# Performance work log

Measured on AMD Instinct MI355X. Metric: run time of the kernel, lower is better.

The kernel has to match this reference:

```python
import jax, jax.numpy as jnp
import numpy as np

B, S, D, H = 4, 1024, 1024, 16
DK = D // H  # f_out = 64


def setup_inputs() -> dict:
    key = jax.random.key(0)
    ks = jax.random.split(key, 20)
    sc = 0.02
    inp = {
        "q": jax.random.normal(ks[0], (B, S, D), jnp.float32),
        "k": jax.random.normal(ks[1], (B, S, D), jnp.float32),
        "v": jax.random.normal(ks[2], (B, S, D), jnp.float32),
        "mask": jnp.ones((B * H, S), jnp.int32),
        # q_lin / k_lin / v_lin: Linear(num_hiddens=D, num_q=D)
        "Wq": jax.random.normal(ks[3], (D, D), jnp.float32) * sc,
        "bq": jnp.zeros((D,), jnp.float32),
        "Wk": jax.random.normal(ks[4], (D, D), jnp.float32) * sc,
        "bk": jnp.zeros((D,), jnp.float32),
        "Wv": jax.random.normal(ks[5], (D, D), jnp.float32) * sc,
        "bv": jnp.zeros((D,), jnp.float32),
        # per-head FeedForward (Linear f_out->f_out + ReLU; dropout is a no-op in eval)
        "Wqf": jax.random.normal(ks[6], (DK, DK), jnp.float32) * sc,
        "bqf": jnp.zeros((DK,), jnp.float32),
        "Wkf": jax.random.normal(ks[7], (DK, DK), jnp.float32) * sc,
        "bkf": jnp.zeros((DK,), jnp.float32),
        "Wvf": jax.random.normal(ks[8], (DK, DK), jnp.float32) * sc,
        "bvf": jnp.zeros((DK,), jnp.float32),
        # out: Linear(f_out, f_out), applied per head before recombining
        "Wo": jax.random.normal(ks[9], (DK, DK), jnp.float32) * sc,
        "bo": jnp.zeros((DK,), jnp.float32),
    }
    return inp


def reference(q, k, v, mask, Wq, bq, Wk, bk, Wv, bv,
              Wqf, bqf, Wkf, bkf, Wvf, bvf, Wo, bo):
    def lin(x, W, b):
        return jnp.einsum("...i,oi->...o", x, W) + b

    def split_heads(x):  # (B,S,D) -> (B*H,S,DK)
        return x.reshape(B, S, H, DK).transpose(0, 2, 1, 3).reshape(B * H, S, DK)

    # projections + head split + per-head FeedForward (Linear -> ReLU)
    Q = jax.nn.relu(lin(split_heads(lin(q, Wq, bq)), Wqf, bqf))
    K = jax.nn.relu(lin(split_heads(lin(k, Wk, bk)), Wkf, bkf))
    V = jax.nn.relu(lin(split_heads(lin(v, Wv, bv)), Wvf, bvf))

    # scaled dot-product attention with padding mask (dropout = identity, eval)
    scores = jnp.einsum("bqd,bkd->bqk", Q, K) / np.sqrt(DK).astype(np.float32)
    scores = jnp.where(mask[:, None, :] == 0, -10000.0, scores)
    attn = jax.nn.softmax(scores, axis=-1)
    out = jnp.einsum("bqk,bkd->bqd", attn, V)  # (B*H,S,DK)

    out = lin(out, Wo, bo)  # per-head output projection (DK -> DK)
    # transpose_output: (B*H,S,DK) -> (B,S,H*DK)
    out = out.reshape(B, H, S, DK).transpose(0, 2, 1, 3).reshape(B, S, H * DK)
    return out
```

## Files before the change

### kernel.cpp

```cpp
#include <hip/hip_runtime.h>
#include <stdint.h>

#define MM 4096
#define SS 1024
#define DD 1024
#define HH 16
#define DKK 64

typedef __bf16 bf16x8 __attribute__((ext_vector_type(8)));
typedef __bf16 bf16x4 __attribute__((ext_vector_type(4)));
typedef float  f32x4  __attribute__((ext_vector_type(4)));

__device__ __forceinline__ void gload_lds16(const void* g, void* l) {
  __builtin_amdgcn_global_load_lds(
      (__attribute__((address_space(1))) void*)g,
      (__attribute__((address_space(3))) void*)l, 16, 0, 0);
}

#define LSW(row, ch) ((row) * 64 + ((((ch) ^ ((row) & 7)) << 3)))

__global__ __launch_bounds__(256) void prep(
    const float* __restrict__ q, const float* __restrict__ k,
    const float* __restrict__ v,
    const float* __restrict__ Wq, const float* __restrict__ bq,
    const float* __restrict__ Wk, const float* __restrict__ bk,
    const float* __restrict__ Wv, const float* __restrict__ bv,
    const float* __restrict__ Wqf, const float* __restrict__ bqf,
    const float* __restrict__ Wkf, const float* __restrict__ bkf,
    const float* __restrict__ Wvf, const float* __restrict__ bvf,
    __bf16* __restrict__ X3, __bf16* __restrict__ Wc3,
    float* __restrict__ bc3) {
  int blk = blockIdx.x;
  if (blk < 6144) {
    int z = blk >> 11;
    int bx = blk & 2047;
    const float* src = (z == 0) ? q : ((z == 1) ? k : v);
    size_t i = ((size_t)bx * 256 + threadIdx.x) * 8;
    float4 a = *(const float4*)(src + i);
    float4 b = *(const float4*)(src + i + 4);
    bf16x8 r;
    r[0] = (__bf16)a.x; r[1] = (__bf16)a.y; r[2] = (__bf16)a.z; r[3] = (__bf16)a.w;
    r[4] = (__bf16)b.x; r[5] = (__bf16)b.y; r[6] = (__bf16)b.z; r[7] = (__bf16)b.w;
    *(bf16x8*)(X3 + (size_t)z * MM * DD + i) = r;
  } else {
    int t = blk - 6144;
    int z = t >> 12;
    int wb = t & 4095;
    int i = (wb & 3) * 256 + threadIdx.x;
    int o = wb >> 2;
    const float* W   = (z == 0) ? Wq  : ((z == 1) ? Wk  : Wv);
    const float* bs  = (z == 0) ? bq  : ((z == 1) ? bk  : bv);
    const float* Wf  = (z == 0) ? Wqf : ((z == 1) ? Wkf : Wvf);
    const float* bf_ = (z == 0) ? bqf : ((z == 1) ? bkf : bvf);
    int h = o >> 6, j = o & 63;
    const float* wfr = Wf + j * DKK;
    float acc = 0.f;
#pragma unroll 8
    for (int d = 0; d < DKK; ++d)
      acc += wfr[d] * W[(size_t)(h * DKK + d) * DD + i];
    Wc3[(size_t)z * DD * DD + (size_t)o * DD + i] = (__bf16)acc;
    if ((wb & 3) == 0 && threadIdx.x == 0) {
      float bb = bf_[j];
      for (int d = 0; d < DKK; ++d) bb += wfr[d] * bs[h * DKK + d];
      bc3[z * DD + o] = bb;
    }
  }
}

__global__ __launch_bounds__(256) void gemm3(const __bf16* __restrict__ X3,
                                             const __bf16* __restrict__ Wc3,
                                             const float* __restrict__ bc3,
                                             __bf16* __restrict__ QKV) {
  __shared__ __bf16 As[128 * 64];
  __shared__ __bf16 Bs[128 * 64];
  const int z = blockIdx.z;
  const __bf16* A  = X3  + (size_t)z * MM * DD;
  const __bf16* Bt = Wc3 + (size_t)z * DD * DD;
  const float* bias = bc3 + z * DD;
  __bf16* C = QKV + (size_t)z * MM * DD;

  const int tid = threadIdx.x;
  const int wave = tid >> 6, lane = tid & 63;
  const int l15 = lane & 15, l4 = lane >> 4;
  const int bm = blockIdx.x * 128;
  const int bn = blockIdx.y * 128;
  const int wr = (wave >> 1) * 64;
  const int wc = (wave & 1) * 64;

  f32x4 acc[4][4] = {};

  const int srow = wave * 8 + (lane >> 3);
  const int scol = (lane & 7) * 8;

  for (int kt = 0; kt < DD; kt += 64) {
    __syncthreads();
#pragma unroll
    for (int j = 0; j < 4; ++j) {
      int row = j * 32 + srow;
      gload_lds16(A  + (size_t)(bm + row) * DD + kt + scol, As + j * 2048 + wave * 512);
      gload_lds16(Bt + (size_t)(bn + row) * DD + kt + scol, Bs + j * 2048 + wave * 512);
    }
    asm volatile("s_waitcnt vmcnt(0)" ::: "memory");
    __syncthreads();
#pragma unroll
    for (int ks = 0; ks < 2; ++ks) {
      bf16x8 af[4], bfr[4];
#pragma unroll
      for (int mi = 0; mi < 4; ++mi)
        af[mi] = *(const bf16x8*)(As + (wr + mi * 16 + l15) * 64 + ks * 32 + l4 * 8);
#pragma unroll
      for (int ni = 0; ni < 4; ++ni)
        bfr[ni] = *(const bf16x8*)(Bs + (wc + ni * 16 + l15) * 64 + ks * 32 + l4 * 8);
#pragma unroll
      for (int mi = 0; mi < 4; ++mi)
#pragma unroll
        for (int ni = 0; ni < 4; ++ni)
          acc[mi][ni] = __builtin_amdgcn_mfma_f32_16x16x32_bf16(af[mi], bfr[ni], acc[mi][ni], 0, 0, 0);
    }
  }

#pragma unroll
  for (int ni = 0; ni < 4; ++ni) {
    int n = bn + wc + ni * 16 + l15;
    float bb = bias[n];
#pragma unroll
    for (int mi = 0; mi < 4; ++mi) {
      if (z != 2) {
#pragma unroll
        for (int r = 0; r < 4; ++r) {
          int m = bm + wr + mi * 16 + l4 * 4 + r;
          float vv = acc[mi][ni][r] + bb;
          vv = vv > 0.f ? vv : 0.f;
          C[(size_t)m * DD + n] = (__bf16)vv;
        }
      } else {
        int m0 = bm + wr + mi * 16 + l4 * 4;
        int b = m0 >> 10, s0 = m0 & 1023;
        int h = n >> 6, dk = n & 63;
        bf16x4 pk;
#pragma unroll
        for (int r = 0; r < 4; ++r) {
          float vv = acc[mi][ni][r] + bb;
          vv = vv > 0.f ? vv : 0.f;
          pk[r] = (__bf16)vv;
        }
        *(bf16x4*)(C + ((size_t)(b * HH + h) * DKK + dk) * SS + s0) = pk;
      }
    }
  }
}

__global__ __launch_bounds__(256) void attn_kernel(
    const __bf16* __restrict__ Q,
    const __bf16* __restrict__ K,
    const __bf16* __restrict__ Vt,
    const int* __restrict__ mask,
    const float* __restrict__ Wo,
    const float* __restrict__ bo,
    float* __restrict__ out)
{
  __shared__ __bf16 Qs[64 * 64];
  __shared__ __bf16 Ks[64 * 64];
  __shared__ __bf16 Vs[64 * 64];
  __shared__ __bf16 Pw[4][16 * 64];
  __shared__ __bf16 Wos[64 * 64];

  const int tid = threadIdx.x;
  const int wave = tid >> 6, lane = tid & 63;
  const int l15 = lane & 15, l4 = lane >> 4;

  const int lin = blockIdx.x + 16 * blockIdx.y;
  const int swz = (lin & 7) * 128 + (lin >> 3);
  const int qt = swz & 15;
  const int bh = swz >> 4;
  const int b = bh >> 4, h = bh & 15;

  const __bf16* Qbase = Q + ((size_t)b * SS + qt * 64) * DD + h * 64;
  const __bf16* Kbase = K + (size_t)b * SS * DD + h * 64;
  const __bf16* Vbase = Vt + (size_t)bh * DKK * SS;

  for (int t = tid; t < 64 * 64; t += 256) {
    int row = t >> 6, col = t & 63;
    Wos[row * 64 + ((((col >> 3) ^ (row & 7)) << 3) | (col & 7))] = (__bf16)Wo[t];
  }

  const int cr = wave * 8 + (lane >> 3);
  const int scol = (((lane & 7) ^ (lane >> 3)) * 8);

#pragma unroll
  for (int j = 0; j < 2; ++j)
    gload_lds16(Qbase + (size_t)(j * 32 + cr) * DD + scol, Qs + j * 2048 + wave * 512);

  f32x4 o_acc[4] = {};
  float mrow[4], lrow[4];
#pragma unroll
  for (int r = 0; r < 4; ++r) { mrow[r] = -1e30f; lrow[r] = 0.f; }

  for (int kt = 0; kt < SS / 64; ++kt) {
    __syncthreads();
#pragma unroll
    for (int j = 0; j < 2; ++j) {
      int row = j * 32 + cr;
      gload_lds16(Kbase + (size_t)(kt * 64 + row) * DD + scol, Ks + j * 2048 + wave * 512);
      gload_lds16(Vbase + (size_t)row * SS + kt * 64 + scol,   Vs + j * 2048 + wave * 512);
    }
    asm volatile("s_waitcnt vmcnt(0)" ::: "memory");
    __syncthreads();

    f32x4 sc[4] = {};
#pragma unroll
    for (int ks = 0; ks < 2; ++ks) {
      bf16x8 aq = *(const bf16x8*)(Qs + LSW(wave * 16 + l15, ks * 4 + l4));
#pragma unroll
      for (int ni = 0; ni < 4; ++ni) {
        bf16x8 kf = *(const bf16x8*)(Ks + LSW(ni * 16 + l15, ks * 4 + l4));
        sc[ni] = __builtin_amdgcn_mfma_f32_16x16x32_bf16(aq, kf, sc[ni], 0, 0, 0);
      }
    }
#pragma unroll
    for (int ni = 0; ni < 4; ++ni) {
      int key = kt * 64 + ni * 16 + l15;
      int mv = mask[bh * SS + key];
#pragma unroll
      for (int r = 0; r < 4; ++r) {
        float s = sc[ni][r] * 0.125f;
        sc[ni][r] = (mv == 0) ? -10000.f : s;
      }
    }
    float alpha[4];
#pragma unroll
    for (int r = 0; r < 4; ++r) {
      float v = fmaxf(fmaxf(sc[0][r], sc[1][r]), fmaxf(sc[2][r], sc[3][r]));
      v = fmaxf(v, __shfl_xor(v, 1));
      v = fmaxf(v, __shfl_xor(v, 2));
      v = fmaxf(v, __shfl_xor(v, 4));
      v = fmaxf(v, __shfl_xor(v, 8));
      float mnew = fmaxf(mrow[r], v);
      alpha[r] = __expf(mrow[r] - mnew);
      mrow[r] = mnew;
      float s = 0.f;
#pragma unroll
      for (int ni = 0; ni < 4; ++ni) {
        float p = __expf(sc[ni][r] - mnew);
        sc[ni][r] = p;
        s += p;
      }
      s += __shfl_xor(s, 1); s += __shfl_xor(s, 2);
      s += __shfl_xor(s, 4); s += __shfl_xor(s, 8);
      lrow[r] = lrow[r] * alpha[r] + s;
    }
#pragma unroll
    for (int ni = 0; ni < 4; ++ni)
#pragma unroll
      for (int r = 0; r < 4; ++r) {
        int row = l4 * 4 + r;
        int ch = 2 * ni + (l15 >> 3);
        Pw[wave][row * 64 + (((ch ^ (row & 7)) << 3) | (l15 & 7))] = (__bf16)sc[ni][r];
      }
    asm volatile("" ::: "memory");
#pragma unroll
    for (int ni = 0; ni < 4; ++ni)
#pragma unroll
      for (int r = 0; r < 4; ++r) o_acc[ni][r] *= alpha[r];
#pragma unroll
    for (int ks = 0; ks < 2; ++ks) {
      bf16x8 ap = *(const bf16x8*)(&Pw[wave][LSW(l15, ks * 4 + l4)]);
#pragma unroll
      for (int ni = 0; ni < 4; ++ni) {
        bf16x8 vf = *(const bf16x8*)(Vs + LSW(ni * 16 + l15, ks * 4 + l4));
        o_acc[ni] = __builtin_amdgcn_mfma_f32_16x16x32_bf16(ap, vf, o_acc[ni], 0, 0, 0);
      }
    }
  }

#pragma unroll
  for (int ni = 0; ni < 4; ++ni)
#pragma unroll
    for (int r = 0; r < 4; ++r) {
      int row = l4 * 4 + r;
      int ch = 2 * ni + (l15 >> 3);
      Pw[wave][row * 64 + (((ch ^ (row & 7)) << 3) | (l15 & 7))] =
          (__bf16)(o_acc[ni][r] / lrow[r]);
    }
  asm volatile("" ::: "memory");
  f32x4 facc[4] = {};
#pragma unroll
  for (int ks = 0; ks < 2; ++ks) {
    bf16x8 ao = *(const bf16x8*)(&Pw[wave][LSW(l15, ks * 4 + l4)]);
#pragma unroll
    for (int ni = 0; ni < 4; ++ni) {
      bf16x8 wf = *(const bf16x8*)(Wos + LSW(ni * 16 + l15, ks * 4 + l4));
      facc[ni] = __builtin_amdgcn_mfma_f32_16x16x32_bf16(ao, wf, facc[ni], 0, 0, 0);
    }
  }
#pragma unroll
  for (int ni = 0; ni < 4; ++ni) {
    int j = ni * 16 + l15;
    float bb = bo[j];
#pragma unroll
    for (int r = 0; r < 4; ++r) {
      int qrow = qt * 64 + wave * 16 + l4 * 4 + r;
      out[((size_t)b * SS + qrow) * DD + h * 64 + j] = facc[ni][r] + bb;
    }
  }
}

extern "C" void kernel_launch(void* const* d_in, const int* in_sizes, int n_in,
                              void* d_out, int out_size, void* d_ws, size_t ws_size,
                              hipStream_t stream) {
  const float* q   = (const float*)d_in[0];
  const float* k   = (const float*)d_in[1];
  const float* v   = (const float*)d_in[2];
  const int*   mask= (const int*)d_in[3];
  const float* Wq  = (const float*)d_in[4];
  const float* bq  = (const float*)d_in[5];
  const float* Wk  = (const float*)d_in[6];
  const float* bk  = (const float*)d_in[7];
  const float* Wv  = (const float*)d_in[8];
  const float* bv  = (const float*)d_in[9];
  const float* Wqf = (const float*)d_in[10];
  const float* bqf = (const float*)d_in[11];
  const float* Wkf = (const float*)d_in[12];
  const float* bkf = (const float*)d_in[13];
  const float* Wvf = (const float*)d_in[14];
  const float* bvf = (const float*)d_in[15];
  const float* Wo  = (const float*)d_in[16];
  const float* bo  = (const float*)d_in[17];
  float* out = (float*)d_out;

  char* p = (char*)d_ws;
  __bf16* X3  = (__bf16*)p; p += (size_t)3 * MM * DD * 2;
  __bf16* Wc3 = (__bf16*)p; p += (size_t)3 * DD * DD * 2;
  __bf16* QKV = (__bf16*)p; p += (size_t)3 * MM * DD * 2;
  float*  bc3 = (float*)p;  p += (size_t)3 * DD * 4;
  if ((size_t)(p - (char*)d_ws) > ws_size) return;

  prep<<<18432, 256, 0, stream>>>(q, k, v, Wq, bq, Wk, bk, Wv, bv,
                                  Wqf, bqf, Wkf, bkf, Wvf, bvf, X3, Wc3, bc3);
  gemm3<<<dim3(32, 8, 3), 256, 0, stream>>>(X3, Wc3, bc3, QKV);
  attn_kernel<<<dim3(16, 64), 256, 0, stream>>>(
      QKV, QKV + (size_t)MM * DD, QKV + (size_t)2 * MM * DD, mask, Wo, bo, out);
}
```

Baseline: 269.5 us.

## Double-buffer K/V in attention with larger Q tiles and restructure weight folding

```diff
diff --git a/kernel.cpp b/kernel.cpp
--- a/kernel.cpp
+++ b/kernel.cpp
@@ -10,6 +10,8 @@
 typedef __bf16 bf16x8 __attribute__((ext_vector_type(8)));
 typedef __bf16 bf16x4 __attribute__((ext_vector_type(4)));
 typedef float  f32x4  __attribute__((ext_vector_type(4)));
+
+#define LOG2E 1.44269504088896340736f
 
 __device__ __forceinline__ void gload_lds16(const void* g, void* l) {
   __builtin_amdgcn_global_load_lds(
@@ -44,25 +46,34 @@
     *(bf16x8*)(X3 + (size_t)z * MM * DD + i) = r;
   } else {
     int t = blk - 6144;
-    int z = t >> 12;
-    int wb = t & 4095;
-    int i = (wb & 3) * 256 + threadIdx.x;
-    int o = wb >> 2;
+    int z = t >> 6;
+    int rem = t & 63;
+    int h = rem >> 2, ic = rem & 3;
     const float* W   = (z == 0) ? Wq  : ((z == 1) ? Wk  : Wv);
     const float* bs  = (z == 0) ? bq  : ((z == 1) ? bk  : bv);
     const float* Wf  = (z == 0) ? Wqf : ((z == 1) ? Wkf : Wvf);
     const float* bf_ = (z == 0) ? bqf : ((z == 1) ? bkf : bvf);
-    int h = o >> 6, j = o & 63;
-    const float* wfr = Wf + j * DKK;
-    float acc = 0.f;
+    int i = ic * 256 + threadIdx.x;
+
+    float acc[64];
+#pragma unroll
+    for (int j = 0; j < 64; ++j) acc[j] = 0.f;
+#pragma unroll 4
+    for (int d = 0; d < 64; ++d) {
+      float wv = W[(size_t)(h * DKK + d) * DD + i];
+#pragma unroll
+      for (int j = 0; j < 64; ++j)
+        acc[j] = fmaf(Wf[j * DKK + d], wv, acc[j]);
+    }
 #pragma unroll 8
-    for (int d = 0; d < DKK; ++d)
-      acc += wfr[d] * W[(size_t)(h * DKK + d) * DD + i];
-    Wc3[(size_t)z * DD * DD + (size_t)o * DD + i] = (__bf16)acc;
-    if ((wb & 3) == 0 && threadIdx.x == 0) {
+    for (int j = 0; j < 64; ++j)
+      Wc3[(size_t)z * DD * DD + (size_t)(h * DKK + j) * DD + i] = (__bf16)acc[j];
+
+    if (ic == 0 && threadIdx.x < 64) {
+      int j = threadIdx.x;
       float bb = bf_[j];
-      for (int d = 0; d < DKK; ++d) bb += wfr[d] * bs[h * DKK + d];
-      bc3[z * DD + o] = bb;
+      for (int d = 0; d < 64; ++d) bb += Wf[j * DKK + d] * bs[h * DKK + d];
+      bc3[z * DD + h * DKK + j] = bb;
     }
   }
 }
@@ -150,7 +161,7 @@
   }
 }
 
-__global__ __launch_bounds__(256) void attn_kernel(
+__global__ __launch_bounds__(512) void attn_kernel(
     const __bf16* __restrict__ Q,
     const __bf16* __restrict__ K,
     const __bf16* __restrict__ Vt,
@@ -159,53 +170,59 @@
     const float* __restrict__ bo,
     float* __restrict__ out)
 {
-  __shared__ __bf16 Qs[64 * 64];
-  __shared__ __bf16 Ks[64 * 64];
-  __shared__ __bf16 Vs[64 * 64];
-  __shared__ __bf16 Pw[4][16 * 64];
+  __shared__ __bf16 Qs[128 * 64];
+  __shared__ __bf16 Ks[2][64 * 64];
+  __shared__ __bf16 Vs[2][64 * 64];
+  __shared__ __bf16 Pw[8][16 * 64];
   __shared__ __bf16 Wos[64 * 64];
 
   const int tid = threadIdx.x;
   const int wave = tid >> 6, lane = tid & 63;
   const int l15 = lane & 15, l4 = lane >> 4;
 
-  const int lin = blockIdx.x + 16 * blockIdx.y;
-  const int swz = (lin & 7) * 128 + (lin >> 3);
-  const int qt = swz & 15;
-  const int bh = swz >> 4;
+  const int lin = blockIdx.x;
+  const int swz = (lin & 7) * 64 + (lin >> 3);
+  const int qt = swz & 7;
+  const int bh = swz >> 3;
   const int b = bh >> 4, h = bh & 15;
 
-  const __bf16* Qbase = Q + ((size_t)b * SS + qt * 64) * DD + h * 64;
+  const __bf16* Qbase = Q + ((size_t)b * SS + qt * 128) * DD + h * 64;
   const __bf16* Kbase = K + (size_t)b * SS * DD + h * 64;
   const __bf16* Vbase = Vt + (size_t)bh * DKK * SS;
 
-  for (int t = tid; t < 64 * 64; t += 256) {
+  for (int t = tid; t < 64 * 64; t += 512) {
     int row = t >> 6, col = t & 63;
     Wos[row * 64 + ((((col >> 3) ^ (row & 7)) << 3) | (col & 7))] = (__bf16)Wo[t];
   }
 
-  const int cr = wave * 8 + (lane >> 3);
-  const int scol = (((lane & 7) ^ (lane >> 3)) * 8);
+  const int lr8 = lane >> 3;
+  const int scol = (((lane & 7) ^ lr8) * 8);
+  const int krow = wave * 8 + lr8;
 
 #pragma unroll
   for (int j = 0; j < 2; ++j)
-    gload_lds16(Qbase + (size_t)(j * 32 + cr) * DD + scol, Qs + j * 2048 + wave * 512);
+    gload_lds16(Qbase + (size_t)(wave * 16 + j * 8 + lr8) * DD + scol,
+                Qs + wave * 1024 + j * 512);
+  gload_lds16(Kbase + (size_t)krow * DD + scol, Ks[0] + wave * 512);
+  gload_lds16(Vbase + (size_t)krow * SS + scol, Vs[0] + wave * 512);
+  asm volatile("s_waitcnt vmcnt(0)" ::: "memory");
+  __syncthreads();
 
   f32x4 o_acc[4] = {};
   float mrow[4], lrow[4];
 #pragma unroll
   for (int r = 0; r < 4; ++r) { mrow[r] = -1e30f; lrow[r] = 0.f; }
 
+  const float SCL = 0.125f * LOG2E;
+
   for (int kt = 0; kt < SS / 64; ++kt) {
-    __syncthreads();
-#pragma unroll
-    for (int j = 0; j < 2; ++j) {
-      int row = j * 32 + cr;
-      gload_lds16(Kbase + (size_t)(kt * 64 + row) * DD + scol, Ks + j * 2048 + wave * 512);
-      gload_lds16(Vbase + (size_t)row * SS + kt * 64 + scol,   Vs + j * 2048 + wave * 512);
-    }
-    asm volatile("s_waitcnt vmcnt(0)" ::: "memory");
-    __syncthreads();
+    const int cur = kt & 1;
+    if (kt < SS / 64 - 1) {
+      gload_lds16(Kbase + (size_t)((kt + 1) * 64 + krow) * DD + scol,
+                  Ks[cur ^ 1] + wave * 512);
+      gload_lds16(Vbase + (size_t)krow * SS + (kt + 1) * 64 + scol,
+                  Vs[cur ^ 1] + wave * 512);
+    }
 
     f32x4 sc[4] = {};
 #pragma unroll
@@ -213,7 +230,7 @@
       bf16x8 aq = *(const bf16x8*)(Qs + LSW(wave * 16 + l15, ks * 4 + l4));
 #pragma unroll
       for (int ni = 0; ni < 4; ++ni) {
-        bf16x8 kf = *(const bf16x8*)(Ks + LSW(ni * 16 + l15, ks * 4 + l4));
+        bf16x8 kf = *(const bf16x8*)(Ks[cur] + LSW(ni * 16 + l15, ks * 4 + l4));
         sc[ni] = __builtin_amdgcn_mfma_f32_16x16x32_bf16(aq, kf, sc[ni], 0, 0, 0);
       }
     }
@@ -223,8 +240,8 @@
       int mv = mask[bh * SS + key];
 #pragma unroll
       for (int r = 0; r < 4; ++r) {
-        float s = sc[ni][r] * 0.125f;
-        sc[ni][r] = (mv == 0) ? -10000.f : s;
+        float s = sc[ni][r] * SCL;
+        sc[ni][r] = (mv == 0) ? (-10000.f * LOG2E) : s;
       }
     }
     float alpha[4];
@@ -236,12 +253,12 @@
       v = fmaxf(v, __shfl_xor(v, 4));
       v = fmaxf(v, __shfl_xor(v, 8));
       float mnew = fmaxf(mrow[r], v);
-      alpha[r] = __expf(mrow[r] - mnew);
+      alpha[r] = __builtin_exp2f(mrow[r] - mnew);
       mrow[r] = mnew;
       float s = 0.f;
 #pragma unroll
       for (int ni = 0; ni < 4; ++ni) {
-        float p = __expf(sc[ni][r] - mnew);
+        float p = __builtin_exp2f(sc[ni][r] - mnew);
         sc[ni][r] = p;
         s += p;
       }
@@ -267,10 +284,12 @@
       bf16x8 ap = *(const bf16x8*)(&Pw[wave][LSW(l15, ks * 4 + l4)]);
 #pragma unroll
       for (int ni = 0; ni < 4; ++ni) {
-        bf16x8 vf = *(const bf16x8*)(Vs + LSW(ni * 16 + l15, ks * 4 + l4));
+        bf16x8 vf = *(const bf16x8*)(Vs[cur] + LSW(ni * 16 + l15, ks * 4 + l4));
         o_acc[ni] = __builtin_amdgcn_mfma_f32_16x16x32_bf16(ap, vf, o_acc[ni], 0, 0, 0);
       }
     }
+    asm volatile("s_waitcnt vmcnt(0)" ::: "memory");
+    __syncthreads();
   }
 
 #pragma unroll
@@ -299,7 +318,7 @@
     float bb = bo[j];
 #pragma unroll
     for (int r = 0; r < 4; ++r) {
-      int qrow = qt * 64 + wave * 16 + l4 * 4 + r;
+      int qrow = qt * 128 + wave * 16 + l4 * 4 + r;
       out[((size_t)b * SS + qrow) * DD + h * 64 + j] = facc[ni][r] + bb;
     }
   }
@@ -335,9 +354,9 @@
   float*  bc3 = (float*)p;  p += (size_t)3 * DD * 4;
   if ((size_t)(p - (char*)d_ws) > ws_size) return;
 
-  prep<<<18432, 256, 0, stream>>>(q, k, v, Wq, bq, Wk, bk, Wv, bv,
-                                  Wqf, bqf, Wkf, bkf, Wvf, bvf, X3, Wc3, bc3);
+  prep<<<6336, 256, 0, stream>>>(q, k, v, Wq, bq, Wk, bk, Wv, bv,
+                                 Wqf, bqf, Wkf, bkf, Wvf, bvf, X3, Wc3, bc3);
   gemm3<<<dim3(32, 8, 3), 256, 0, stream>>>(X3, Wc3, bc3, QKV);
-  attn_kernel<<<dim3(16, 64), 256, 0, stream>>>(
+  attn_kernel<<<512, 512, 0, stream>>>(
       QKV, QKV + (size_t)MM * DD, QKV + (size_t)2 * MM * DD, mask, Wo, bo, out);
 }
```

Measured after the change: 352.8 us. 30.9% more time.
